# Kernel optimization log

Hardware: AMD Instinct MI355X
Metric: run time of the kernel (lower is better)

The kernel has to match this reference:

```python
import jax, jax.numpy as jnp
import numpy as np

ALPHA = 0.2  # LeakyReLU negative slope


def _head(x, W, b, a, eye):
    # x: [B,N,F], W: [F,D], a: [2D,1], eye: [N,N] identity
    h = x @ W + b                                   # [B,N,D]
    D = W.shape[1]
    # additive attention: score[i,j] = leakyrelu(a_l . h_i + a_r . h_j)
    s = jax.nn.leaky_relu(h @ a[:D] + jnp.swapaxes(h @ a[D:], 1, 2), ALPHA)  # [B,N,N]
    s = jnp.where(eye > 0, -jnp.inf, s)             # mask diagonal (adj_identity)
    p = jax.nn.softmax(s, axis=-1) + eye            # softmax then add identity
    return jax.nn.elu(p @ h)                        # [B,N,D]


def setup_inputs() -> dict:
    key = jax.random.key(0)
    ks = jax.random.split(key, 16)
    B, N, F_IN, HID, HEADS = 8, 2048, 256, 256, 2
    D = HID // HEADS
    inp = {
        "x": jax.random.normal(ks[0], (B, N, F_IN), dtype=jnp.float32),
        "edges": jax.random.randint(ks[1], (B, N), 0, N, dtype=jnp.int64),
    }
    i = 2
    for layer in range(2):
        fin = F_IN if layer == 0 else HID
        for head in range(HEADS):
            inp[f"W_{layer}_{head}"] = jax.random.normal(ks[i], (fin, D), dtype=jnp.float32) * (1.0 / np.sqrt(fin)); i += 1
            inp[f"b_{layer}_{head}"] = jnp.zeros((D,), dtype=jnp.float32)
            inp[f"a_{layer}_{head}"] = jax.random.normal(ks[i], (2 * D, 1), dtype=jnp.float32) * 0.1; i += 1
    return inp


def reference(x, edges, W_0_0, b_0_0, a_0_0, W_0_1, b_0_1, a_0_1,
              W_1_0, b_1_0, a_1_0, W_1_1, b_1_1, a_1_1):
    N = x.shape[1]
    eye = jnp.eye(N, dtype=x.dtype)
    layers = [
        [(W_0_0, b_0_0, a_0_0), (W_0_1, b_0_1, a_0_1)],
        [(W_1_0, b_1_0, a_1_0), (W_1_1, b_1_1, a_1_1)],
    ]
    for heads in layers:
        x = jnp.concatenate([_head(x, W, b, a, eye) for (W, b, a) in heads], axis=-1)
    return x
```

## Files before the change

kernel.cpp:

```cpp
#include <hip/hip_runtime.h>
#include <math.h>

#define ALPHA_SLOPE 0.2f

typedef _Float16 f16;
typedef f16 f16x4 __attribute__((ext_vector_type(4)));
typedef f16 f16x8 __attribute__((ext_vector_type(8)));
typedef float f32x4 __attribute__((ext_vector_type(4)));

constexpr int B_ = 8, N = 2048, D = 128, H = 2;
constexpr int C2 = H * D;
constexpr int M_ = B_ * N;
constexpr int NCH = 32;
constexpr int CHL = N / NCH;

__device__ __forceinline__ float lrelu(float x) { return fmaxf(x, ALPHA_SLOPE * x); }

__global__ __launch_bounds__(256) void cvt_kernel(
    const float* __restrict__ x, f16* __restrict__ xh,
    const float* __restrict__ W00, const float* __restrict__ W01,
    const float* __restrict__ W10, const float* __restrict__ W11,
    f16* __restrict__ WcT)
{
    const int t = threadIdx.x;
    if (blockIdx.x < 4096) {
        const int idx = (blockIdx.x * 256 + t) * 4;
        const float4 v = *(const float4*)&x[idx];
        f16x4 o; o[0] = (f16)v.x; o[1] = (f16)v.y; o[2] = (f16)v.z; o[3] = (f16)v.w;
        *(f16x4*)&xh[idx] = o;
    } else {
        const int w = blockIdx.x - 4096;
#pragma unroll
        for (int p = 0; p < 4; ++p) {
            const int pair = w * 4 + p;
            const int layer = pair >> 8, c = pair & 255;
            const float* __restrict__ W0 = layer ? W10 : W00;
            const float* __restrict__ W1 = layer ? W11 : W01;
            const float v = (c < D) ? W0[t * D + c] : W1[t * D + (c - D)];
            WcT[(size_t)layer * C2 * C2 + c * C2 + t] = (f16)v;
        }
    }
}

__global__ __launch_bounds__(256) void gemm_lr_kernel(
    const f16* __restrict__ xh, const f16* __restrict__ Wl,
    const float* __restrict__ b0, const float* __restrict__ b1,
    const float* __restrict__ a0, const float* __restrict__ a1,
    f16* __restrict__ h,
    float* __restrict__ l0, float* __restrict__ r0,
    float* __restrict__ l1, float* __restrict__ r1)
{
    __shared__ f16 hts[32][C2 + 8];
    const int t = threadIdx.x;
    const int row0 = blockIdx.x * 32;
#pragma unroll
    for (int p = 0; p < 4; ++p) {
        const int q = p * 256 + t;
        const int row = q >> 5, cc = q & 31;
        *(f16x8*)&hts[row][cc * 8] = *(const f16x8*)&xh[(size_t)(row0 + row) * C2 + cc * 8];
    }
    __syncthreads();
    const int w = t >> 6, l = t & 63;
    const int fm = l & 15, fk = (l >> 4) * 8;
    f32x4 acc[2][4] = {};
#pragma unroll
    for (int ks = 0; ks < 8; ++ks) {
        f16x8 af[2], bf[4];
#pragma unroll
        for (int rt = 0; rt < 2; ++rt)
            af[rt] = *(const f16x8*)&hts[rt * 16 + fm][ks * 32 + fk];
#pragma unroll
        for (int ct = 0; ct < 4; ++ct) {
            const int col = w * 64 + ct * 16 + fm;
            bf[ct] = *(const f16x8*)&Wl[(size_t)col * C2 + ks * 32 + fk];
        }
#pragma unroll
        for (int rt = 0; rt < 2; ++rt)
#pragma unroll
            for (int ct = 0; ct < 4; ++ct)
                acc[rt][ct] = __builtin_amdgcn_mfma_f32_16x16x32_f16(af[rt], bf[ct], acc[rt][ct], 0, 0, 0);
    }
    __syncthreads();
#pragma unroll
    for (int rt = 0; rt < 2; ++rt)
#pragma unroll
        for (int ct = 0; ct < 4; ++ct) {
            const int col = w * 64 + ct * 16 + fm;
            const float bias = (col < D) ? b0[col] : b1[col - D];
#pragma unroll
            for (int q = 0; q < 4; ++q) {
                const int row = rt * 16 + (l >> 4) * 4 + q;
                hts[row][col] = (f16)(acc[rt][ct][q] + bias);
            }
        }
    __syncthreads();
#pragma unroll
    for (int p = 0; p < 4; ++p) {
        const int q = p * 256 + t;
        const int row = q >> 5, cc = q & 31;
        *(f16x8*)&h[(size_t)(row0 + row) * C2 + cc * 8] = *(const f16x8*)&hts[row][cc * 8];
    }
    const int lrow = t >> 3;
    const int oct = t & 7;
    const float* __restrict__ ab = (oct >= 4) ? a1 : a0;
    float lv = 0.f, rv = 0.f;
#pragma unroll
    for (int c4 = 0; c4 < 8; ++c4) {
        const int cc = (c4 + oct) & 7;
        const int col = oct * 32 + cc * 4;
        const int cih = (oct & 3) * 32 + cc * 4;
        const f16x4 hf = *(const f16x4*)&hts[lrow][col];
        const float4 alv = *(const float4*)&ab[cih];
        const float4 arv = *(const float4*)&ab[128 + cih];
        const float h0 = (float)hf[0], h1 = (float)hf[1], h2 = (float)hf[2], h3 = (float)hf[3];
        lv += h0 * alv.x + h1 * alv.y + h2 * alv.z + h3 * alv.w;
        rv += h0 * arv.x + h1 * arv.y + h2 * arv.z + h3 * arv.w;
    }
    lv += __shfl_xor(lv, 1, 64); lv += __shfl_xor(lv, 2, 64);
    rv += __shfl_xor(rv, 1, 64); rv += __shfl_xor(rv, 2, 64);
    const int grow = row0 + lrow;
    if (oct == 0) { l0[grow] = lv; r0[grow] = rv; }
    else if (oct == 4) { l1[grow] = lv; r1[grow] = rv; }
}

__global__ __launch_bounds__(256) void rank_kernel(
    const float* __restrict__ r0, const float* __restrict__ r1,
    const float* __restrict__ l0, const float* __restrict__ l1,
    float* __restrict__ rs_s, int* __restrict__ perm, int* __restrict__ kout)
{
    const int bh = blockIdx.y;
    const float* __restrict__ r = ((bh & 1) ? r1 : r0) + (size_t)(bh >> 1) * N;
    const float* __restrict__ lp = ((bh & 1) ? l1 : l0) + (size_t)(bh >> 1) * N;
    __shared__ float rl[N];
    __shared__ int scnt[4][64], sk2[4][64];
    const int t = threadIdx.x;
    for (int j = t; j < N; j += 256) rl[j] = r[j];
    __syncthreads();
    const int el = t & 63;
    const int q = t >> 6;
    const int e = blockIdx.x * 64 + el;
    const float re = rl[e];
    const float thr = -lp[e];
    const int qm = blockIdx.x >> 3;
    int cnt = 0, k2 = 0;
    const int jlo = q * 512, jhi = jlo + 512;
    if (q < qm) {
        for (int j = jlo; j < jhi; j += 4) {
            const float4 v = *(const float4*)&rl[j];
            cnt += (v.x >= re) + (v.y >= re) + (v.z >= re) + (v.w >= re);
            k2  += (v.x >= thr) + (v.y >= thr) + (v.z >= thr) + (v.w >= thr);
        }
    } else if (q > qm) {
        for (int j = jlo; j < jhi; j += 4) {
            const float4 v = *(const float4*)&rl[j];
            cnt += (v.x > re) + (v.y > re) + (v.z > re) + (v.w > re);
            k2  += (v.x >= thr) + (v.y >= thr) + (v.z >= thr) + (v.w >= thr);
        }
    } else {
        for (int j = jlo; j < jhi; j += 4) {
            const float4 v = *(const float4*)&rl[j];
            cnt += (v.x > re) || (v.x == re && (j + 0) < e);
            cnt += (v.y > re) || (v.y == re && (j + 1) < e);
            cnt += (v.z > re) || (v.z == re && (j + 2) < e);
            cnt += (v.w > re) || (v.w == re && (j + 3) < e);
            k2  += (v.x >= thr) + (v.y >= thr) + (v.z >= thr) + (v.w >= thr);
        }
    }
    scnt[q][el] = cnt; sk2[q][el] = k2;
    __syncthreads();
    if (t < 64) {
        const int c = scnt[0][t] + scnt[1][t] + scnt[2][t] + scnt[3][t];
        const int kk = sk2[0][t] + sk2[1][t] + sk2[2][t] + sk2[3][t];
        const int eg = blockIdx.x * 64 + t;
        const size_t g = (size_t)bh * N;
        rs_s[g + c] = rl[eg];
        perm[g + c] = eg;
        kout[g + eg] = kk;
    }
}

__global__ __launch_bounds__(256) void scanA_kernel(
    const f16* __restrict__ h, const int* __restrict__ perm,
    const float* __restrict__ rs_s,
    f16* __restrict__ PA, f16* __restrict__ PB,
    float* __restrict__ SAloc, float* __restrict__ SBloc,
    float* __restrict__ totA, float* __restrict__ totB,
    float* __restrict__ stA, float* __restrict__ stB)
{
    __shared__ f16 hs[CHL][D];
    __shared__ int pj[CHL];
    __shared__ float wA[CHL], wB[CHL];
    __shared__ float buf[2 * CHL];
    const int chunk = blockIdx.x, bh = blockIdx.y;
    const int b = bh >> 1, head = bh & 1;
    const int t = threadIdx.x;
    const size_t g = (size_t)bh * N + chunk * CHL;
    const float c1 = rs_s[(size_t)bh * N];
    if (t < CHL) {
        pj[t] = perm[g + t];
        const float rr = rs_s[g + t];
        const float eA = __expf(rr - c1);
        const float eB = __expf(0.2f * (rr - c1));
        wA[t] = eA; wB[t] = eB;
        buf[t] = eA;
    } else if (t < 2 * CHL) {
        const float rr = rs_s[g + (CHL - 1 - (t - CHL))];
        buf[t] = __expf(0.2f * (rr - c1));
    }
    __syncthreads();
    const int li = t & (CHL - 1);
#pragma unroll
    for (int off = 1; off < CHL; off <<= 1) {
        const float v = (t < 2 * CHL && li >= off) ? buf[t - off] : 0.f;
        __syncthreads();
        if (t < 2 * CHL && li >= off) buf[t] += v;
        __syncthreads();
    }
    if (t < CHL) SAloc[g + t] = buf[t];
    else if (t < 2 * CHL) SBloc[g + (CHL - 1 - li)] = buf[t];
    if (t == CHL - 1) stA[bh * NCH + chunk] = buf[CHL - 1];
    if (t == 2 * CHL - 1) stB[bh * NCH + chunk] = buf[2 * CHL - 1];
#pragma unroll
    for (int p = 0; p < 4; ++p) {
        const int q = p * 256 + t;
        const int row = q >> 4, c8 = q & 15;
        const f16* src = h + (size_t)(b * N + pj[row]) * C2 + head * D;
        *(f16x8*)&hs[row][c8 * 8] = *(const f16x8*)&src[c8 * 8];
    }
    __syncthreads();
    if (t < D) {
        const int d = t;
        float acc = 0.f;
        for (int j = 0; j < CHL; ++j) {
            acc = fmaf(wA[j], (float)hs[j][d], acc);
            PA[(g + j) * D + d] = (f16)acc;
        }
        totA[(size_t)(bh * NCH + chunk) * D + d] = acc;
    } else {
        const int d = t - D;
        float acc = 0.f;
        for (int jj = 0; jj < CHL; ++jj) {
            const int j = CHL - 1 - jj;
            acc = fmaf(wB[j], (float)hs[j][d], acc);
            PB[(g + j) * D + d] = (f16)acc;
        }
        totB[(size_t)(bh * NCH + chunk) * D + d] = acc;
    }
}

__global__ __launch_bounds__(256) void out_kernel(
    const f16* __restrict__ h,
    const float* __restrict__ l0v, const float* __restrict__ l1v,
    const float* __restrict__ r0v, const float* __restrict__ r1v,
    const int* __restrict__ perm, const float* __restrict__ rs_s,
    const int* __restrict__ kout,
    const float* __restrict__ SAloc, const float* __restrict__ SBloc,
    const float* __restrict__ stA, const float* __restrict__ stB,
    const float* __restrict__ totA, const float* __restrict__ totB,
    const f16* __restrict__ PA, const f16* __restrict__ PB,
    float* __restrict__ out_f32, f16* __restrict__ out_f16, const int final_layer)
{
    __shared__ float ldsA[NCH][D];
    __shared__ float ldsB[NCH][D];
    __shared__ float lsA[NCH], lsB[NCH];
    const int head = blockIdx.y, b = blockIdx.z;
    const int bh = b * H + head;
    const float* __restrict__ lv = (head ? l1v : l0v) + (size_t)b * N;
    const float* __restrict__ rv = (head ? r1v : r0v) + (size_t)b * N;
    const int t = threadIdx.x;
    const size_t gb = (size_t)bh * N;

#pragma unroll
    for (int p = 0; p < 4; ++p) {
        const int idx = p * 256 + t;
        const int ch = idx >> 5, c4 = idx & 31;
        *(float4*)&ldsA[ch][c4 * 4] = *(const float4*)&totA[(size_t)(bh * NCH + ch) * D + c4 * 4];
        *(float4*)&ldsB[ch][c4 * 4] = *(const float4*)&totB[(size_t)(bh * NCH + ch) * D + c4 * 4];
    }
    if (t < NCH) lsA[t] = stA[bh * NCH + t];
    else if (t < 2 * NCH) lsB[t - NCH] = stB[bh * NCH + (t - NCH)];
    __syncthreads();
    if (t < D) {
        const int d = t;
        float acc = 0.f;
        for (int q = 0; q < NCH; ++q) {
            const float tmp = ldsA[q][d];
            ldsA[q][d] = acc;
            acc += tmp;
        }
    } else {
        const int d = t - D;
        float acc = 0.f;
        for (int q = NCH - 1; q >= 0; --q) {
            const float tmp = ldsB[q][d];
            ldsB[q][d] = acc;
            acc += tmp;
        }
    }
    if (t == 0) {
        float a = 0.f;
        for (int q = 0; q < NCH; ++q) { const float tmp = lsA[q]; lsA[q] = a; a += tmp; }
    } else if (t == 1) {
        float a = 0.f;
        for (int q = NCH - 1; q >= 0; --q) { const float tmp = lsB[q]; lsB[q] = a; a += tmp; }
    }
    __syncthreads();

    const int i = blockIdx.x * 16 + (t >> 4);
    const int c0 = (t & 15) * 8;
    const float li = lv[i];
    const float ri = rv[i];
    const float rmx1 = rs_s[gb];
    const float rmx2 = rs_s[gb + 1];
    const int rdx = perm[gb];
    const float rmx = (i == rdx) ? rmx2 : rmx1;
    const float m = lrelu(li + rmx);
    const float alpha = __expf(li + rmx1 - m);
    const float beta = __expf(0.2f * (li + rmx1) - m);
    const float diag = __expf(lrelu(li + ri) - m);

    const int k = kout[gb + i];
    const float SAk = (k > 0) ? (lsA[(k - 1) >> 6] + SAloc[gb + k - 1]) : 0.f;
    const float SBk = (k < N) ? (lsB[k >> 6] + SBloc[gb + k]) : 0.f;
    const float Z = fmaf(alpha, SAk, beta * SBk) - diag;
    const float invZ = 1.f / Z;

    float pa[8] = {}, pb[8] = {};
    if (k > 0) {
        const int kk = k - 1, ch = kk >> 6;
        const f16x8 v = *(const f16x8*)&PA[(gb + kk) * D + c0];
#pragma unroll
        for (int q = 0; q < 8; ++q) pa[q] = (float)v[q] + ldsA[ch][c0 + q];
    }
    if (k < N) {
        const int ch = k >> 6;
        const f16x8 v = *(const f16x8*)&PB[(gb + k) * D + c0];
#pragma unroll
        for (int q = 0; q < 8; ++q) pb[q] = (float)v[q] + ldsB[ch][c0 + q];
    }

    const f16x8 hraw = *(const f16x8*)&h[(size_t)(b * N + i) * C2 + head * D + c0];
    float o[8];
#pragma unroll
    for (int q = 0; q < 8; ++q) {
        const float hv = (float)hraw[q];
        const float num = alpha * pa[q] + beta * pb[q] - diag * hv;
        float v = fmaf(num, invZ, hv);
        o[q] = v > 0.f ? v : (__expf(v) - 1.f);
    }
    const size_t oidx = (size_t)(b * N + i) * C2 + head * D + c0;
    if (final_layer) {
        *(float4*)&out_f32[oidx] = make_float4(o[0], o[1], o[2], o[3]);
        *(float4*)&out_f32[oidx + 4] = make_float4(o[4], o[5], o[6], o[7]);
    } else {
        f16x8 ov;
#pragma unroll
        for (int q = 0; q < 8; ++q) ov[q] = (f16)o[q];
        *(f16x8*)&out_f16[oidx] = ov;
    }
}

extern "C" void kernel_launch(void* const* d_in, const int* in_sizes, int n_in,
                              void* d_out, int out_size, void* d_ws, size_t ws_size,
                              hipStream_t stream)
{
    float* ws = (float*)d_ws;
    size_t off = 0;
    f16* xh = (f16*)(ws + off);   off += (size_t)M_ * C2 / 2;
    f16* WcT = (f16*)(ws + off);  off += (size_t)C2 * C2;
    f16* h = (f16*)(ws + off);    off += (size_t)M_ * C2 / 2;
    float* l0 = ws + off;         off += (size_t)B_ * N;
    float* r0 = ws + off;         off += (size_t)B_ * N;
    float* l1 = ws + off;         off += (size_t)B_ * N;
    float* r1 = ws + off;         off += (size_t)B_ * N;
    float* rs_s = ws + off;       off += (size_t)16 * N;
    int* perm = (int*)(ws + off); off += (size_t)16 * N;
    int* kout = (int*)(ws + off); off += (size_t)16 * N;
    float* SAloc = ws + off;      off += (size_t)16 * N;
    float* SBloc = ws + off;      off += (size_t)16 * N;
    f16* PA = (f16*)(ws + off);   off += (size_t)16 * N * D / 2;
    f16* PB = (f16*)(ws + off);   off += (size_t)16 * N * D / 2;
    float* totA = ws + off;       off += (size_t)16 * NCH * D;
    float* totB = ws + off;       off += (size_t)16 * NCH * D;
    float* stA = ws + off;        off += (size_t)16 * NCH;
    float* stB = ws + off;        off += (size_t)16 * NCH;

    cvt_kernel<<<4096 + 128, 256, 0, stream>>>(
        (const float*)d_in[0], xh,
        (const float*)d_in[2], (const float*)d_in[5],
        (const float*)d_in[8], (const float*)d_in[11], WcT);

    for (int layer = 0; layer < 2; ++layer) {
        const int base = 2 + layer * 6;
        const float* b0 = (const float*)d_in[base + 1];
        const float* a0 = (const float*)d_in[base + 2];
        const float* b1 = (const float*)d_in[base + 4];
        const float* a1 = (const float*)d_in[base + 5];

        gemm_lr_kernel<<<M_ / 32, 256, 0, stream>>>(
            xh, WcT + (size_t)layer * C2 * C2, b0, b1, a0, a1, h, l0, r0, l1, r1);
        rank_kernel<<<dim3(N / 64, B_ * H), 256, 0, stream>>>(
            r0, r1, l0, l1, rs_s, perm, kout);
        scanA_kernel<<<dim3(NCH, B_ * H), 256, 0, stream>>>(
            h, perm, rs_s, PA, PB, SAloc, SBloc, totA, totB, stA, stB);
        out_kernel<<<dim3(N / 16, H, B_), 256, 0, stream>>>(
            h, l0, l1, r0, r1, perm, rs_s, kout, SAloc, SBloc, stA, stB,
            totA, totB, PA, PB, (float*)d_out, xh, layer == 1 ? 1 : 0);
    }
}
```

Measured before the change: 208.6 us.

## Fuse fp32 input conversion into GEMM, halve GEMM tile rows, split scan over D

The layer-0 GEMM now reads the fp32 input and converts it to fp16 inside the kernel, so the separate x conversion pass and its round trip through memory are dropped. The GEMM block handles 16 rows instead of 32, doubling the block count, and scanA splits the feature dimension across two blocks per chunk. Both grid changes raise parallelism, at the cost of less B-operand reuse in the GEMM and a duplicated gather and exponent computation in scanA.

```diff
diff --git a/kernel.cpp b/kernel.cpp
--- a/kernel.cpp
+++ b/kernel.cpp
@@ -16,111 +16,112 @@
 
 __device__ __forceinline__ float lrelu(float x) { return fmaxf(x, ALPHA_SLOPE * x); }
 
-__global__ __launch_bounds__(256) void cvt_kernel(
-    const float* __restrict__ x, f16* __restrict__ xh,
+__global__ __launch_bounds__(256) void cvtW_kernel(
     const float* __restrict__ W00, const float* __restrict__ W01,
     const float* __restrict__ W10, const float* __restrict__ W11,
     f16* __restrict__ WcT)
 {
     const int t = threadIdx.x;
-    if (blockIdx.x < 4096) {
-        const int idx = (blockIdx.x * 256 + t) * 4;
-        const float4 v = *(const float4*)&x[idx];
-        f16x4 o; o[0] = (f16)v.x; o[1] = (f16)v.y; o[2] = (f16)v.z; o[3] = (f16)v.w;
-        *(f16x4*)&xh[idx] = o;
-    } else {
-        const int w = blockIdx.x - 4096;
-#pragma unroll
-        for (int p = 0; p < 4; ++p) {
-            const int pair = w * 4 + p;
-            const int layer = pair >> 8, c = pair & 255;
-            const float* __restrict__ W0 = layer ? W10 : W00;
-            const float* __restrict__ W1 = layer ? W11 : W01;
-            const float v = (c < D) ? W0[t * D + c] : W1[t * D + (c - D)];
-            WcT[(size_t)layer * C2 * C2 + c * C2 + t] = (f16)v;
-        }
+    const int w = blockIdx.x;
+#pragma unroll
+    for (int p = 0; p < 4; ++p) {
+        const int pair = w * 4 + p;
+        const int layer = pair >> 8, c = pair & 255;
+        const float* __restrict__ W0 = layer ? W10 : W00;
+        const float* __restrict__ W1 = layer ? W11 : W01;
+        const float v = (c < D) ? W0[t * D + c] : W1[t * D + (c - D)];
+        WcT[(size_t)layer * C2 * C2 + c * C2 + t] = (f16)v;
     }
 }
 
 __global__ __launch_bounds__(256) void gemm_lr_kernel(
-    const f16* __restrict__ xh, const f16* __restrict__ Wl,
+    const float* __restrict__ x32, const f16* __restrict__ xh,
+    const f16* __restrict__ Wl,
     const float* __restrict__ b0, const float* __restrict__ b1,
     const float* __restrict__ a0, const float* __restrict__ a1,
     f16* __restrict__ h,
     float* __restrict__ l0, float* __restrict__ r0,
-    float* __restrict__ l1, float* __restrict__ r1)
-{
-    __shared__ f16 hts[32][C2 + 8];
+    float* __restrict__ l1, float* __restrict__ r1,
+    const int use32)
+{
+    __shared__ f16 hts[16][C2 + 8];
     const int t = threadIdx.x;
-    const int row0 = blockIdx.x * 32;
-#pragma unroll
-    for (int p = 0; p < 4; ++p) {
-        const int q = p * 256 + t;
-        const int row = q >> 5, cc = q & 31;
-        *(f16x8*)&hts[row][cc * 8] = *(const f16x8*)&xh[(size_t)(row0 + row) * C2 + cc * 8];
+    const int row0 = blockIdx.x * 16;
+    if (use32) {
+#pragma unroll
+        for (int p = 0; p < 4; ++p) {
+            const int q = p * 256 + t;
+            const int row = q >> 6, c4 = q & 63;
+            const float4 v = *(const float4*)&x32[(size_t)(row0 + row) * C2 + c4 * 4];
+            f16x4 o; o[0] = (f16)v.x; o[1] = (f16)v.y; o[2] = (f16)v.z; o[3] = (f16)v.w;
+            *(f16x4*)&hts[row][c4 * 4] = o;
+        }
+    } else {
+#pragma unroll
+        for (int p = 0; p < 2; ++p) {
+            const int q = p * 256 + t;
+            const int row = q >> 5, cc = q & 31;
+            *(f16x8*)&hts[row][cc * 8] = *(const f16x8*)&xh[(size_t)(row0 + row) * C2 + cc * 8];
+        }
     }
     __syncthreads();
     const int w = t >> 6, l = t & 63;
     const int fm = l & 15, fk = (l >> 4) * 8;
-    f32x4 acc[2][4] = {};
+    f32x4 acc[4] = {};
 #pragma unroll
     for (int ks = 0; ks < 8; ++ks) {
-        f16x8 af[2], bf[4];
-#pragma unroll
-        for (int rt = 0; rt < 2; ++rt)
-            af[rt] = *(const f16x8*)&hts[rt * 16 + fm][ks * 32 + fk];
+        f16x8 af, bf[4];
+        af = *(const f16x8*)&hts[fm][ks * 32 + fk];
 #pragma unroll
         for (int ct = 0; ct < 4; ++ct) {
             const int col = w * 64 + ct * 16 + fm;
             bf[ct] = *(const f16x8*)&Wl[(size_t)col * C2 + ks * 32 + fk];
         }
 #pragma unroll
-        for (int rt = 0; rt < 2; ++rt)
-#pragma unroll
-            for (int ct = 0; ct < 4; ++ct)
-                acc[rt][ct] = __builtin_amdgcn_mfma_f32_16x16x32_f16(af[rt], bf[ct], acc[rt][ct], 0, 0, 0);
-    }
-    __syncthreads();
-#pragma unroll
-    for (int rt = 0; rt < 2; ++rt)
-#pragma unroll
-        for (int ct = 0; ct < 4; ++ct) {
-            const int col = w * 64 + ct * 16 + fm;
-            const float bias = (col < D) ? b0[col] : b1[col - D];
-#pragma unroll
-            for (int q = 0; q < 4; ++q) {
-                const int row = rt * 16 + (l >> 4) * 4 + q;
-                hts[row][col] = (f16)(acc[rt][ct][q] + bias);
-            }
-        }
-    __syncthreads();
-#pragma unroll
-    for (int p = 0; p < 4; ++p) {
+        for (int ct = 0; ct < 4; ++ct)
+            acc[ct] = __builtin_amdgcn_mfma_f32_16x16x32_f16(af, bf[ct], acc[ct], 0, 0, 0);
+    }
+    __syncthreads();
+#pragma unroll
+    for (int ct = 0; ct < 4; ++ct) {
+        const int col = w * 64 + ct * 16 + fm;
+        const float bias = (col < D) ? b0[col] : b1[col - D];
+#pragma unroll
+        for (int q = 0; q < 4; ++q) {
+            const int row = (l >> 4) * 4 + q;
+            hts[row][col] = (f16)(acc[ct][q] + bias);
+        }
+    }
+    __syncthreads();
+#pragma unroll
+    for (int p = 0; p < 2; ++p) {
         const int q = p * 256 + t;
         const int row = q >> 5, cc = q & 31;
         *(f16x8*)&h[(size_t)(row0 + row) * C2 + cc * 8] = *(const f16x8*)&hts[row][cc * 8];
     }
-    const int lrow = t >> 3;
-    const int oct = t & 7;
-    const float* __restrict__ ab = (oct >= 4) ? a1 : a0;
-    float lv = 0.f, rv = 0.f;
-#pragma unroll
-    for (int c4 = 0; c4 < 8; ++c4) {
-        const int cc = (c4 + oct) & 7;
-        const int col = oct * 32 + cc * 4;
-        const int cih = (oct & 3) * 32 + cc * 4;
-        const f16x4 hf = *(const f16x4*)&hts[lrow][col];
-        const float4 alv = *(const float4*)&ab[cih];
-        const float4 arv = *(const float4*)&ab[128 + cih];
-        const float h0 = (float)hf[0], h1 = (float)hf[1], h2 = (float)hf[2], h3 = (float)hf[3];
-        lv += h0 * alv.x + h1 * alv.y + h2 * alv.z + h3 * alv.w;
-        rv += h0 * arv.x + h1 * arv.y + h2 * arv.z + h3 * arv.w;
-    }
-    lv += __shfl_xor(lv, 1, 64); lv += __shfl_xor(lv, 2, 64);
-    rv += __shfl_xor(rv, 1, 64); rv += __shfl_xor(rv, 2, 64);
-    const int grow = row0 + lrow;
-    if (oct == 0) { l0[grow] = lv; r0[grow] = rv; }
-    else if (oct == 4) { l1[grow] = lv; r1[grow] = rv; }
+    if (t < 128) {
+        const int lrow = t >> 3;
+        const int oct = t & 7;
+        const float* __restrict__ ab = (oct >= 4) ? a1 : a0;
+        float lv = 0.f, rv = 0.f;
+#pragma unroll
+        for (int c4 = 0; c4 < 8; ++c4) {
+            const int cc = (c4 + oct) & 7;
+            const int col = oct * 32 + cc * 4;
+            const int cih = (oct & 3) * 32 + cc * 4;
+            const f16x4 hf = *(const f16x4*)&hts[lrow][col];
+            const float4 alv = *(const float4*)&ab[cih];
+            const float4 arv = *(const float4*)&ab[128 + cih];
+            const float h0 = (float)hf[0], h1 = (float)hf[1], h2 = (float)hf[2], h3 = (float)hf[3];
+            lv += h0 * alv.x + h1 * alv.y + h2 * alv.z + h3 * alv.w;
+            rv += h0 * arv.x + h1 * arv.y + h2 * arv.z + h3 * arv.w;
+        }
+        lv += __shfl_xor(lv, 1, 64); lv += __shfl_xor(lv, 2, 64);
+        rv += __shfl_xor(rv, 1, 64); rv += __shfl_xor(rv, 2, 64);
+        const int grow = row0 + lrow;
+        if (oct == 0) { l0[grow] = lv; r0[grow] = rv; }
+        else if (oct == 4) { l1[grow] = lv; r1[grow] = rv; }
+    }
 }
 
 __global__ __launch_bounds__(256) void rank_kernel(
@@ -187,11 +188,11 @@
     float* __restrict__ totA, float* __restrict__ totB,
     float* __restrict__ stA, float* __restrict__ stB)
 {
-    __shared__ f16 hs[CHL][D];
+    __shared__ f16 hs[CHL][64];
     __shared__ int pj[CHL];
     __shared__ float wA[CHL], wB[CHL];
     __shared__ float buf[2 * CHL];
-    const int chunk = blockIdx.x, bh = blockIdx.y;
+    const int chunk = blockIdx.x, dh = blockIdx.y, bh = blockIdx.z;
     const int b = bh >> 1, head = bh & 1;
     const int t = threadIdx.x;
     const size_t g = (size_t)bh * N + chunk * CHL;
@@ -202,49 +203,51 @@
         const float eA = __expf(rr - c1);
         const float eB = __expf(0.2f * (rr - c1));
         wA[t] = eA; wB[t] = eB;
-        buf[t] = eA;
-    } else if (t < 2 * CHL) {
+        if (dh == 0) buf[t] = eA;
+    } else if (t < 2 * CHL && dh == 0) {
         const float rr = rs_s[g + (CHL - 1 - (t - CHL))];
         buf[t] = __expf(0.2f * (rr - c1));
     }
     __syncthreads();
-    const int li = t & (CHL - 1);
-#pragma unroll
-    for (int off = 1; off < CHL; off <<= 1) {
-        const float v = (t < 2 * CHL && li >= off) ? buf[t - off] : 0.f;
-        __syncthreads();
-        if (t < 2 * CHL && li >= off) buf[t] += v;
-        __syncthreads();
-    }
-    if (t < CHL) SAloc[g + t] = buf[t];
-    else if (t < 2 * CHL) SBloc[g + (CHL - 1 - li)] = buf[t];
-    if (t == CHL - 1) stA[bh * NCH + chunk] = buf[CHL - 1];
-    if (t == 2 * CHL - 1) stB[bh * NCH + chunk] = buf[2 * CHL - 1];
-#pragma unroll
-    for (int p = 0; p < 4; ++p) {
+    if (dh == 0) {
+        const int li = t & (CHL - 1);
+#pragma unroll
+        for (int off = 1; off < CHL; off <<= 1) {
+            const float v = (t < 2 * CHL && li >= off) ? buf[t - off] : 0.f;
+            __syncthreads();
+            if (t < 2 * CHL && li >= off) buf[t] += v;
+            __syncthreads();
+        }
+        if (t < CHL) SAloc[g + t] = buf[t];
+        else if (t < 2 * CHL) SBloc[g + (CHL - 1 - li)] = buf[t];
+        if (t == CHL - 1) stA[bh * NCH + chunk] = buf[CHL - 1];
+        if (t == 2 * CHL - 1) stB[bh * NCH + chunk] = buf[2 * CHL - 1];
+    }
+#pragma unroll
+    for (int p = 0; p < 2; ++p) {
         const int q = p * 256 + t;
-        const int row = q >> 4, c8 = q & 15;
-        const f16* src = h + (size_t)(b * N + pj[row]) * C2 + head * D;
+        const int row = q >> 3, c8 = q & 7;
+        const f16* __restrict__ src = h + (size_t)(b * N + pj[row]) * C2 + head * D + dh * 64;
         *(f16x8*)&hs[row][c8 * 8] = *(const f16x8*)&src[c8 * 8];
     }
     __syncthreads();
-    if (t < D) {
+    if (t < 64) {
         const int d = t;
         float acc = 0.f;
         for (int j = 0; j < CHL; ++j) {
             acc = fmaf(wA[j], (float)hs[j][d], acc);
-            PA[(g + j) * D + d] = (f16)acc;
-        }
-        totA[(size_t)(bh * NCH + chunk) * D + d] = acc;
-    } else {
-        const int d = t - D;
+            PA[(g + j) * D + dh * 64 + d] = (f16)acc;
+        }
+        totA[(size_t)(bh * NCH + chunk) * D + dh * 64 + d] = acc;
+    } else if (t < 128) {
+        const int d = t - 64;
         float acc = 0.f;
         for (int jj = 0; jj < CHL; ++jj) {
             const int j = CHL - 1 - jj;
             acc = fmaf(wB[j], (float)hs[j][d], acc);
-            PB[(g + j) * D + d] = (f16)acc;
-        }
-        totB[(size_t)(bh * NCH + chunk) * D + d] = acc;
+            PB[(g + j) * D + dh * 64 + d] = (f16)acc;
+        }
+        totB[(size_t)(bh * NCH + chunk) * D + dh * 64 + d] = acc;
     }
 }
 
@@ -385,8 +388,9 @@
     float* stA = ws + off;        off += (size_t)16 * NCH;
     float* stB = ws + off;        off += (size_t)16 * NCH;
 
-    cvt_kernel<<<4096 + 128, 256, 0, stream>>>(
-        (const float*)d_in[0], xh,
+    const float* x32 = (const float*)d_in[0];
+
+    cvtW_kernel<<<128, 256, 0, stream>>>(
         (const float*)d_in[2], (const float*)d_in[5],
         (const float*)d_in[8], (const float*)d_in[11], WcT);
 
@@ -397,11 +401,12 @@
         const float* b1 = (const float*)d_in[base + 4];
         const float* a1 = (const float*)d_in[base + 5];
 
-        gemm_lr_kernel<<<M_ / 32, 256, 0, stream>>>(
-            xh, WcT + (size_t)layer * C2 * C2, b0, b1, a0, a1, h, l0, r0, l1, r1);
+        gemm_lr_kernel<<<M_ / 16, 256, 0, stream>>>(
+            x32, xh, WcT + (size_t)layer * C2 * C2, b0, b1, a0, a1,
+            h, l0, r0, l1, r1, layer == 0 ? 1 : 0);
         rank_kernel<<<dim3(N / 64, B_ * H), 256, 0, stream>>>(
             r0, r1, l0, l1, rs_s, perm, kout);
-        scanA_kernel<<<dim3(NCH, B_ * H), 256, 0, stream>>>(
+        scanA_kernel<<<dim3(NCH, 2, B_ * H), 256, 0, stream>>>(
             h, perm, rs_s, PA, PB, SAloc, SBloc, totA, totB, stA, stB);
         out_kernel<<<dim3(N / 16, H, B_), 256, 0, stream>>>(
             h, l0, l1, r0, r1, perm, rs_s, kout, SAloc, SBloc, stA, stB,
```

Result: slower. 218.1 us (+4.5%).

## Fuse input fp16 conversion into GEMM and hoist chunk-offset scan out of output kernel

Applied to the files above, without the earlier changes.

The layer-0 GEMM now reads the fp32 input directly and converts it to fp16 while staging into shared memory. This removes the separate pass over x that wrote an fp16 copy and the extra read of that copy. The per-block prefix scan over chunk totals in out_kernel is moved into a small scanOff kernel that runs once per (batch, head), so the 256 output blocks per head no longer each redo the 32x128 scan and its shared-memory syncs. In exchange there is one more kernel launch, and out_kernel now fetches the offsets from global memory instead of LDS.

```diff
diff --git a/kernel.cpp b/kernel.cpp
--- a/kernel.cpp
+++ b/kernel.cpp
@@ -16,48 +16,53 @@
 
 __device__ __forceinline__ float lrelu(float x) { return fmaxf(x, ALPHA_SLOPE * x); }
 
-__global__ __launch_bounds__(256) void cvt_kernel(
-    const float* __restrict__ x, f16* __restrict__ xh,
+__global__ __launch_bounds__(256) void cvtW_kernel(
     const float* __restrict__ W00, const float* __restrict__ W01,
     const float* __restrict__ W10, const float* __restrict__ W11,
     f16* __restrict__ WcT)
 {
     const int t = threadIdx.x;
-    if (blockIdx.x < 4096) {
-        const int idx = (blockIdx.x * 256 + t) * 4;
-        const float4 v = *(const float4*)&x[idx];
-        f16x4 o; o[0] = (f16)v.x; o[1] = (f16)v.y; o[2] = (f16)v.z; o[3] = (f16)v.w;
-        *(f16x4*)&xh[idx] = o;
-    } else {
-        const int w = blockIdx.x - 4096;
-#pragma unroll
-        for (int p = 0; p < 4; ++p) {
-            const int pair = w * 4 + p;
-            const int layer = pair >> 8, c = pair & 255;
-            const float* __restrict__ W0 = layer ? W10 : W00;
-            const float* __restrict__ W1 = layer ? W11 : W01;
-            const float v = (c < D) ? W0[t * D + c] : W1[t * D + (c - D)];
-            WcT[(size_t)layer * C2 * C2 + c * C2 + t] = (f16)v;
-        }
+    const int w = blockIdx.x;
+#pragma unroll
+    for (int p = 0; p < 4; ++p) {
+        const int pair = w * 4 + p;
+        const int layer = pair >> 8, c = pair & 255;
+        const float* __restrict__ W0 = layer ? W10 : W00;
+        const float* __restrict__ W1 = layer ? W11 : W01;
+        const float v = (c < D) ? W0[t * D + c] : W1[t * D + (c - D)];
+        WcT[(size_t)layer * C2 * C2 + c * C2 + t] = (f16)v;
     }
 }
 
 __global__ __launch_bounds__(256) void gemm_lr_kernel(
-    const f16* __restrict__ xh, const f16* __restrict__ Wl,
+    const float* __restrict__ x32, const f16* __restrict__ xh,
+    const f16* __restrict__ Wl,
     const float* __restrict__ b0, const float* __restrict__ b1,
     const float* __restrict__ a0, const float* __restrict__ a1,
     f16* __restrict__ h,
     float* __restrict__ l0, float* __restrict__ r0,
-    float* __restrict__ l1, float* __restrict__ r1)
+    float* __restrict__ l1, float* __restrict__ r1,
+    const int use32)
 {
     __shared__ f16 hts[32][C2 + 8];
     const int t = threadIdx.x;
     const int row0 = blockIdx.x * 32;
-#pragma unroll
-    for (int p = 0; p < 4; ++p) {
-        const int q = p * 256 + t;
-        const int row = q >> 5, cc = q & 31;
-        *(f16x8*)&hts[row][cc * 8] = *(const f16x8*)&xh[(size_t)(row0 + row) * C2 + cc * 8];
+    if (use32) {
+#pragma unroll
+        for (int p = 0; p < 8; ++p) {
+            const int q = p * 256 + t;
+            const int row = q >> 6, c4 = q & 63;
+            const float4 v = *(const float4*)&x32[(size_t)(row0 + row) * C2 + c4 * 4];
+            f16x4 o; o[0] = (f16)v.x; o[1] = (f16)v.y; o[2] = (f16)v.z; o[3] = (f16)v.w;
+            *(f16x4*)&hts[row][c4 * 4] = o;
+        }
+    } else {
+#pragma unroll
+        for (int p = 0; p < 4; ++p) {
+            const int q = p * 256 + t;
+            const int row = q >> 5, cc = q & 31;
+            *(f16x8*)&hts[row][cc * 8] = *(const f16x8*)&xh[(size_t)(row0 + row) * C2 + cc * 8];
+        }
     }
     __syncthreads();
     const int w = t >> 6, l = t & 63;
@@ -248,6 +253,45 @@
     }
 }
 
+__global__ __launch_bounds__(256) void scanOff_kernel(
+    const float* __restrict__ totA, const float* __restrict__ totB,
+    const float* __restrict__ stA, const float* __restrict__ stB,
+    float* __restrict__ AOff, float* __restrict__ BOffS,
+    float* __restrict__ lsAg, float* __restrict__ lsBg)
+{
+    const int bh = blockIdx.x;
+    const int t = threadIdx.x;
+    const size_t base = (size_t)bh * NCH;
+    if (t < D) {
+        const int d = t;
+        float acc = 0.f;
+#pragma unroll
+        for (int ch = 0; ch < NCH; ++ch) {
+            const float tmp = totA[(base + ch) * D + d];
+            AOff[(base + ch) * D + d] = acc;
+            acc += tmp;
+        }
+    } else {
+        const int d = t - D;
+        float acc = 0.f;
+#pragma unroll
+        for (int ch = NCH - 1; ch >= 0; --ch) {
+            const float tmp = totB[(base + ch) * D + d];
+            BOffS[(base + ch) * D + d] = acc;
+            acc += tmp;
+        }
+    }
+    if (t == 0) {
+        float a = 0.f;
+#pragma unroll
+        for (int q = 0; q < NCH; ++q) { const float tmp = stA[base + q]; lsAg[base + q] = a; a += tmp; }
+    } else if (t == 64) {
+        float a = 0.f;
+#pragma unroll
+        for (int q = NCH - 1; q >= 0; --q) { const float tmp = stB[base + q]; lsBg[base + q] = a; a += tmp; }
+    }
+}
+
 __global__ __launch_bounds__(256) void out_kernel(
     const f16* __restrict__ h,
     const float* __restrict__ l0v, const float* __restrict__ l1v,
@@ -255,56 +299,18 @@
     const int* __restrict__ perm, const float* __restrict__ rs_s,
     const int* __restrict__ kout,
     const float* __restrict__ SAloc, const float* __restrict__ SBloc,
-    const float* __restrict__ stA, const float* __restrict__ stB,
-    const float* __restrict__ totA, const float* __restrict__ totB,
+    const float* __restrict__ lsAg, const float* __restrict__ lsBg,
+    const float* __restrict__ AOff, const float* __restrict__ BOffS,
     const f16* __restrict__ PA, const f16* __restrict__ PB,
     float* __restrict__ out_f32, f16* __restrict__ out_f16, const int final_layer)
 {
-    __shared__ float ldsA[NCH][D];
-    __shared__ float ldsB[NCH][D];
-    __shared__ float lsA[NCH], lsB[NCH];
     const int head = blockIdx.y, b = blockIdx.z;
     const int bh = b * H + head;
     const float* __restrict__ lv = (head ? l1v : l0v) + (size_t)b * N;
     const float* __restrict__ rv = (head ? r1v : r0v) + (size_t)b * N;
     const int t = threadIdx.x;
     const size_t gb = (size_t)bh * N;
-
-#pragma unroll
-    for (int p = 0; p < 4; ++p) {
-        const int idx = p * 256 + t;
-        const int ch = idx >> 5, c4 = idx & 31;
-        *(float4*)&ldsA[ch][c4 * 4] = *(const float4*)&totA[(size_t)(bh * NCH + ch) * D + c4 * 4];
-        *(float4*)&ldsB[ch][c4 * 4] = *(const float4*)&totB[(size_t)(bh * NCH + ch) * D + c4 * 4];
-    }
-    if (t < NCH) lsA[t] = stA[bh * NCH + t];
-    else if (t < 2 * NCH) lsB[t - NCH] = stB[bh * NCH + (t - NCH)];
-    __syncthreads();
-    if (t < D) {
-        const int d = t;
-        float acc = 0.f;
-        for (int q = 0; q < NCH; ++q) {
-            const float tmp = ldsA[q][d];
-            ldsA[q][d] = acc;
-            acc += tmp;
-        }
-    } else {
-        const int d = t - D;
-        float acc = 0.f;
-        for (int q = NCH - 1; q >= 0; --q) {
-            const float tmp = ldsB[q][d];
-            ldsB[q][d] = acc;
-            acc += tmp;
-        }
-    }
-    if (t == 0) {
-        float a = 0.f;
-        for (int q = 0; q < NCH; ++q) { const float tmp = lsA[q]; lsA[q] = a; a += tmp; }
-    } else if (t == 1) {
-        float a = 0.f;
-        for (int q = NCH - 1; q >= 0; --q) { const float tmp = lsB[q]; lsB[q] = a; a += tmp; }
-    }
-    __syncthreads();
+    const size_t obase = (size_t)bh * NCH;
 
     const int i = blockIdx.x * 16 + (t >> 4);
     const int c0 = (t & 15) * 8;
@@ -320,8 +326,8 @@
     const float diag = __expf(lrelu(li + ri) - m);
 
     const int k = kout[gb + i];
-    const float SAk = (k > 0) ? (lsA[(k - 1) >> 6] + SAloc[gb + k - 1]) : 0.f;
-    const float SBk = (k < N) ? (lsB[k >> 6] + SBloc[gb + k]) : 0.f;
+    const float SAk = (k > 0) ? (lsAg[obase + ((k - 1) >> 6)] + SAloc[gb + k - 1]) : 0.f;
+    const float SBk = (k < N) ? (lsBg[obase + (k >> 6)] + SBloc[gb + k]) : 0.f;
     const float Z = fmaf(alpha, SAk, beta * SBk) - diag;
     const float invZ = 1.f / Z;
 
@@ -329,14 +335,22 @@
     if (k > 0) {
         const int kk = k - 1, ch = kk >> 6;
         const f16x8 v = *(const f16x8*)&PA[(gb + kk) * D + c0];
-#pragma unroll
-        for (int q = 0; q < 8; ++q) pa[q] = (float)v[q] + ldsA[ch][c0 + q];
+        const float4 o0 = *(const float4*)&AOff[(obase + ch) * D + c0];
+        const float4 o1 = *(const float4*)&AOff[(obase + ch) * D + c0 + 4];
+        pa[0] = (float)v[0] + o0.x; pa[1] = (float)v[1] + o0.y;
+        pa[2] = (float)v[2] + o0.z; pa[3] = (float)v[3] + o0.w;
+        pa[4] = (float)v[4] + o1.x; pa[5] = (float)v[5] + o1.y;
+        pa[6] = (float)v[6] + o1.z; pa[7] = (float)v[7] + o1.w;
     }
     if (k < N) {
         const int ch = k >> 6;
         const f16x8 v = *(const f16x8*)&PB[(gb + k) * D + c0];
-#pragma unroll
-        for (int q = 0; q < 8; ++q) pb[q] = (float)v[q] + ldsB[ch][c0 + q];
+        const float4 o0 = *(const float4*)&BOffS[(obase + ch) * D + c0];
+        const float4 o1 = *(const float4*)&BOffS[(obase + ch) * D + c0 + 4];
+        pb[0] = (float)v[0] + o0.x; pb[1] = (float)v[1] + o0.y;
+        pb[2] = (float)v[2] + o0.z; pb[3] = (float)v[3] + o0.w;
+        pb[4] = (float)v[4] + o1.x; pb[5] = (float)v[5] + o1.y;
+        pb[6] = (float)v[6] + o1.z; pb[7] = (float)v[7] + o1.w;
     }
 
     const f16x8 hraw = *(const f16x8*)&h[(size_t)(b * N + i) * C2 + head * D + c0];
@@ -384,9 +398,14 @@
     float* totB = ws + off;       off += (size_t)16 * NCH * D;
     float* stA = ws + off;        off += (size_t)16 * NCH;
     float* stB = ws + off;        off += (size_t)16 * NCH;
-
-    cvt_kernel<<<4096 + 128, 256, 0, stream>>>(
-        (const float*)d_in[0], xh,
+    float* AOff = ws + off;       off += (size_t)16 * NCH * D;
+    float* BOffS = ws + off;      off += (size_t)16 * NCH * D;
+    float* lsAg = ws + off;       off += (size_t)16 * NCH;
+    float* lsBg = ws + off;       off += (size_t)16 * NCH;
+
+    const float* x32 = (const float*)d_in[0];
+
+    cvtW_kernel<<<128, 256, 0, stream>>>(
         (const float*)d_in[2], (const float*)d_in[5],
         (const float*)d_in[8], (const float*)d_in[11], WcT);
 
@@ -398,13 +417,16 @@
         const float* a1 = (const float*)d_in[base + 5];
 
         gemm_lr_kernel<<<M_ / 32, 256, 0, stream>>>(
-            xh, WcT + (size_t)layer * C2 * C2, b0, b1, a0, a1, h, l0, r0, l1, r1);
+            x32, xh, WcT + (size_t)layer * C2 * C2, b0, b1, a0, a1,
+            h, l0, r0, l1, r1, layer == 0 ? 1 : 0);
         rank_kernel<<<dim3(N / 64, B_ * H), 256, 0, stream>>>(
             r0, r1, l0, l1, rs_s, perm, kout);
         scanA_kernel<<<dim3(NCH, B_ * H), 256, 0, stream>>>(
             h, perm, rs_s, PA, PB, SAloc, SBloc, totA, totB, stA, stB);
+        scanOff_kernel<<<B_ * H, 256, 0, stream>>>(
+            totA, totB, stA, stB, AOff, BOffS, lsAg, lsBg);
         out_kernel<<<dim3(N / 16, H, B_), 256, 0, stream>>>(
-            h, l0, l1, r0, r1, perm, rs_s, kout, SAloc, SBloc, stA, stB,
-            totA, totB, PA, PB, (float*)d_out, xh, layer == 1 ? 1 : 0);
-    }
-}
+            h, l0, l1, r0, r1, perm, rs_s, kout, SAloc, SBloc, lsAg, lsBg,
+            AOff, BOffS, PA, PB, (float*)d_out, xh, layer == 1 ? 1 : 0);
+    }
+}
```

Measured after the change: 199.8 us. -4.3%, faster.
